# Optimization experiments

Hardware: AMD Instinct MI355X
Metric: run time of the kernel (lower is better)

## Reference

```python
import jax, jax.numpy as jnp
import numpy as np

BATCH = 1_000_000
NUM_KDE = 500_000
RKHS = 20
OUT = 128
NUM_NODES = 100_000


def setup_inputs() -> dict:
    key = jax.random.key(0)
    ks = jax.random.split(key, 9)
    src = jax.random.randint(ks[0], (BATCH,), 0, NUM_NODES, dtype=jnp.int64 if jax.config.read('jax_enable_x64') else jnp.int32)
    dst = jax.random.randint(ks[1], (BATCH,), 0, NUM_NODES, dtype=src.dtype)
    t_diff = jax.random.uniform(ks[2], (BATCH,), dtype=jnp.float32) * 1000.0
    kde_idx = jax.random.randint(ks[3], (BATCH,), 0, NUM_KDE, dtype=src.dtype)
    kde_mask = jax.random.randint(ks[4], (BATCH,), 0, 2) == 1
    kde_table = jax.random.normal(ks[5], (NUM_KDE, RKHS), dtype=jnp.float32)
    W_proj = jax.random.normal(ks[6], (OUT, RKHS), dtype=jnp.float32) * (1.0 / np.sqrt(RKHS))
    b_proj = jnp.zeros((OUT,), dtype=jnp.float32)
    W_fb = jax.random.normal(ks[7], (OUT, 1), dtype=jnp.float32)
    b_fb = jax.random.normal(ks[8], (OUT,), dtype=jnp.float32)
    return {
        'src': src, 'dst': dst, 't_diff': t_diff,
        'kde_idx': kde_idx, 'kde_mask': kde_mask, 'kde_table': kde_table,
        'W_proj': W_proj, 'b_proj': b_proj, 'W_fb': W_fb, 'b_fb': b_fb,
    }


def reference(src, dst, t_diff, kde_idx, kde_mask, kde_table, W_proj, b_proj, W_fb, b_fb):
    # Gather KDE vectors for every edge (miss rows gather a dummy row, masked out below).
    kde_vecs = kde_table[kde_idx]                       # [B, RKHS]
    # rkhs_projection: Linear(RKHS -> OUT)
    kde_out = jnp.einsum('br,or->bo', kde_vecs, W_proj) + b_proj   # [B, OUT]
    # fallback_encoder: cos(Linear(1 -> OUT))
    fb_out = jnp.cos(t_diff[:, None] * W_fb[:, 0][None, :] + b_fb)  # [B, OUT]
    return jnp.where(kde_mask[:, None], kde_out, fb_out)
```

## Files before the change

kernel.cpp:

```cpp
#include <hip/hip_runtime.h>
#include <hip/hip_bf16.h>

#define BATCH_N 1000000
#define RKHS_N 20
#define OUT_N 128
#define ROWS_PER_WAVE 16
#define ROWS_PER_BLOCK 64

__global__ void kde_probe(const unsigned char* __restrict__ mask,
                          const unsigned short* __restrict__ td,
                          unsigned int* __restrict__ cfg)
{
    int i = blockIdx.x * blockDim.x + threadIdx.x;
    unsigned int bits = 0;
    if ((i & 3) != 0 && mask[i] != 0) bits |= 1u;
    if (td[2 * i] & 0x8000u)          bits |= 2u;
    unsigned long long m1 = __ballot(bits & 1u);
    unsigned long long m2 = __ballot(bits & 2u);
    if ((threadIdx.x & 63) == 0) {
        unsigned int v = (m1 ? 1u : 0u) | (m2 ? 2u : 0u);
        if (v) atomicOr(cfg, v);
    }
}

template<bool BF16>
__device__ __forceinline__ float ldf(const void* p, long long i)
{
    if constexpr (BF16) {
        return __bfloat162float(((const __hip_bfloat16*)p)[i]);
    } else {
        return ((const float*)p)[i];
    }
}

template<bool BF16, bool MASK8>
__device__ __forceinline__ void run_impl(const void* __restrict__ t_diff,
                                         const int* __restrict__ kde_idx,
                                         const void* __restrict__ kde_mask,
                                         const void* __restrict__ kde_table,
                                         const void* __restrict__ W_proj,
                                         const void* __restrict__ b_proj,
                                         const void* __restrict__ W_fb,
                                         const void* __restrict__ b_fb,
                                         void* __restrict__ out)
{
    const int tid  = threadIdx.x;
    const int wave = tid >> 6;
    const int lane = tid & 63;
    const int o0   = lane * 2;

    float w0[RKHS_N], w1[RKHS_N];
#pragma unroll
    for (int r = 0; r < RKHS_N; ++r) {
        w0[r] = ldf<BF16>(W_proj, (long long)o0 * RKHS_N + r);
        w1[r] = ldf<BF16>(W_proj, (long long)(o0 + 1) * RKHS_N + r);
    }
    const float bp0 = ldf<BF16>(b_proj, o0), bp1 = ldf<BF16>(b_proj, o0 + 1);
    const float wf0 = ldf<BF16>(W_fb,  o0), wf1 = ldf<BF16>(W_fb,  o0 + 1);
    const float bb0 = ldf<BF16>(b_fb,  o0), bb1 = ldf<BF16>(b_fb,  o0 + 1);

    const long long base = (long long)blockIdx.x * ROWS_PER_BLOCK
                         + (long long)wave * ROWS_PER_WAVE;

    int idxs[ROWS_PER_WAVE];
    int mvs[ROWS_PER_WAVE];
#pragma unroll
    for (int r = 0; r < ROWS_PER_WAVE; ++r) {
        long long b = base + r;
        int idx = kde_idx[b];
        int m = MASK8 ? (int)((const unsigned char*)kde_mask)[b]
                      : ((const int*)kde_mask)[b];
        idxs[r] = __builtin_amdgcn_readfirstlane(idx);
        mvs[r]  = __builtin_amdgcn_readfirstlane(m);
    }

#pragma unroll
    for (int r = 0; r < ROWS_PER_WAVE; ++r) {
        long long b = base + r;
        float2 res;
        if (mvs[r]) {
            long long voff = (long long)idxs[r] * RKHS_N;
            float a0 = bp0, a1 = bp1;
#pragma unroll
            for (int k = 0; k < RKHS_N; ++k) {
                float v = ldf<BF16>(kde_table, voff + k);
                a0 = fmaf(v, w0[k], a0);
                a1 = fmaf(v, w1[k], a1);
            }
            res.x = a0; res.y = a1;
        } else {
            float t = ldf<BF16>(t_diff, b);
            res.x = __cosf(fmaf(t, wf0, bb0));
            res.y = __cosf(fmaf(t, wf1, bb1));
        }
        long long widx = b * (OUT_N / 2) + lane;
        if constexpr (BF16) {
            __hip_bfloat162 pk;
            pk.x = __float2bfloat16(res.x);
            pk.y = __float2bfloat16(res.y);
            unsigned int ub;
            __builtin_memcpy(&ub, &pk, 4);
            __builtin_nontemporal_store(ub, (unsigned int*)out + widx);
        } else {
            unsigned long long uv;
            __builtin_memcpy(&uv, &res, 8);
            __builtin_nontemporal_store(uv, (unsigned long long*)out + widx);
        }
    }
}

__global__ __launch_bounds__(256)
void kde_main(const void* __restrict__ t_diff,
              const int* __restrict__ kde_idx,
              const void* __restrict__ kde_mask,
              const void* __restrict__ kde_table,
              const void* __restrict__ W_proj,
              const void* __restrict__ b_proj,
              const void* __restrict__ W_fb,
              const void* __restrict__ b_fb,
              void* __restrict__ out,
              const unsigned int* __restrict__ cfg)
{
    const unsigned int c = *cfg;
    if (c & 2u) {
        if (c & 1u) run_impl<false, true >(t_diff, kde_idx, kde_mask, kde_table, W_proj, b_proj, W_fb, b_fb, out);
        else        run_impl<false, false>(t_diff, kde_idx, kde_mask, kde_table, W_proj, b_proj, W_fb, b_fb, out);
    } else {
        if (c & 1u) run_impl<true,  true >(t_diff, kde_idx, kde_mask, kde_table, W_proj, b_proj, W_fb, b_fb, out);
        else        run_impl<true,  false>(t_diff, kde_idx, kde_mask, kde_table, W_proj, b_proj, W_fb, b_fb, out);
    }
}

extern "C" void kernel_launch(void* const* d_in, const int* in_sizes, int n_in,
                              void* d_out, int out_size, void* d_ws, size_t ws_size,
                              hipStream_t stream)
{
    const void* t_diff    = d_in[2];
    const int*  kde_idx   = (const int*)d_in[3];
    const void* kde_mask  = d_in[4];
    const void* kde_table = d_in[5];
    const void* W_proj    = d_in[6];
    const void* b_proj    = d_in[7];
    const void* W_fb      = d_in[8];
    const void* b_fb      = d_in[9];

    unsigned int* cfg = (unsigned int*)d_ws;
    hipMemsetAsync(cfg, 0, sizeof(unsigned int), stream);
    kde_probe<<<256, 256, 0, stream>>>((const unsigned char*)kde_mask,
                                       (const unsigned short*)t_diff, cfg);
    kde_main<<<BATCH_N / ROWS_PER_BLOCK, 256, 0, stream>>>(
        t_diff, kde_idx, kde_mask, kde_table, W_proj, b_proj, W_fb, b_fb,
        d_out, cfg);
}
```

Before: 709.0 us.

## Stage KDE row gathers cooperatively through LDS with packed bf16 loads

Instead of each lane redundantly loading all table elements for a row through per-lane scalar loads, each wave gathers its 16 rows' KDE vectors cooperatively as dwords into LDS, then reads them back with vector LDS loads. Mask, t_diff and weights are loaded as packed dwords and unpacked from bf16 by bit shifts. This aims to cut gather latency and load instruction count, but it gathers rows even for masked-out edges and relies on in-wave LDS ordering without a barrier.

```diff
diff --git a/kernel.cpp b/kernel.cpp
--- a/kernel.cpp
+++ b/kernel.cpp
@@ -4,8 +4,10 @@
 #define BATCH_N 1000000
 #define RKHS_N 20
 #define OUT_N 128
-#define ROWS_PER_WAVE 16
-#define ROWS_PER_BLOCK 64
+#define RPW 16
+#define WAVES 4
+#define ROWS_PER_BLOCK (RPW * WAVES)
+#define GRID_N (BATCH_N / ROWS_PER_BLOCK)
 
 __global__ void kde_probe(const unsigned char* __restrict__ mask,
                           const unsigned short* __restrict__ td,
@@ -23,14 +25,11 @@
     }
 }
 
-template<bool BF16>
-__device__ __forceinline__ float ldf(const void* p, long long i)
-{
-    if constexpr (BF16) {
-        return __bfloat162float(((const __hip_bfloat16*)p)[i]);
-    } else {
-        return ((const float*)p)[i];
-    }
+__device__ __forceinline__ float bflo(unsigned int w) {
+    return __uint_as_float(w << 16);
+}
+__device__ __forceinline__ float bfhi(unsigned int w) {
+    return __uint_as_float(w & 0xffff0000u);
 }
 
 template<bool BF16, bool MASK8>
@@ -42,69 +41,126 @@
                                          const void* __restrict__ b_proj,
                                          const void* __restrict__ W_fb,
                                          const void* __restrict__ b_fb,
-                                         void* __restrict__ out)
-{
+                                         void* __restrict__ out,
+                                         unsigned int* __restrict__ lds)
+{
+    constexpr int DW   = BF16 ? 10 : 20;
+    constexpr int LDSW = BF16 ? 12 : 20;
+    constexpr int TOT  = RPW * DW;
+
     const int tid  = threadIdx.x;
     const int wave = tid >> 6;
     const int lane = tid & 63;
-    const int o0   = lane * 2;
+    const int base = blockIdx.x * ROWS_PER_BLOCK + wave * RPW;
 
     float w0[RKHS_N], w1[RKHS_N];
-#pragma unroll
-    for (int r = 0; r < RKHS_N; ++r) {
-        w0[r] = ldf<BF16>(W_proj, (long long)o0 * RKHS_N + r);
-        w1[r] = ldf<BF16>(W_proj, (long long)(o0 + 1) * RKHS_N + r);
-    }
-    const float bp0 = ldf<BF16>(b_proj, o0), bp1 = ldf<BF16>(b_proj, o0 + 1);
-    const float wf0 = ldf<BF16>(W_fb,  o0), wf1 = ldf<BF16>(W_fb,  o0 + 1);
-    const float bb0 = ldf<BF16>(b_fb,  o0), bb1 = ldf<BF16>(b_fb,  o0 + 1);
-
-    const long long base = (long long)blockIdx.x * ROWS_PER_BLOCK
-                         + (long long)wave * ROWS_PER_WAVE;
-
-    int idxs[ROWS_PER_WAVE];
-    int mvs[ROWS_PER_WAVE];
-#pragma unroll
-    for (int r = 0; r < ROWS_PER_WAVE; ++r) {
-        long long b = base + r;
-        int idx = kde_idx[b];
-        int m = MASK8 ? (int)((const unsigned char*)kde_mask)[b]
-                      : ((const int*)kde_mask)[b];
-        idxs[r] = __builtin_amdgcn_readfirstlane(idx);
-        mvs[r]  = __builtin_amdgcn_readfirstlane(m);
-    }
-
-#pragma unroll
-    for (int r = 0; r < ROWS_PER_WAVE; ++r) {
-        long long b = base + r;
-        float2 res;
-        if (mvs[r]) {
-            long long voff = (long long)idxs[r] * RKHS_N;
+    float bp0, bp1, wf0, wf1, bb0, bb1;
+    if constexpr (BF16) {
+        const unsigned int* wp = (const unsigned int*)W_proj;
+#pragma unroll
+        for (int d = 0; d < 10; ++d) {
+            unsigned int a = wp[lane * 20 + d];
+            unsigned int b = wp[lane * 20 + 10 + d];
+            w0[2 * d] = bflo(a); w0[2 * d + 1] = bfhi(a);
+            w1[2 * d] = bflo(b); w1[2 * d + 1] = bfhi(b);
+        }
+        unsigned int v;
+        v = ((const unsigned int*)b_proj)[lane]; bp0 = bflo(v); bp1 = bfhi(v);
+        v = ((const unsigned int*)W_fb)[lane];   wf0 = bflo(v); wf1 = bfhi(v);
+        v = ((const unsigned int*)b_fb)[lane];   bb0 = bflo(v); bb1 = bfhi(v);
+    } else {
+        const float* wp = (const float*)W_proj;
+#pragma unroll
+        for (int k = 0; k < RKHS_N; ++k) {
+            w0[k] = wp[(2 * lane) * RKHS_N + k];
+            w1[k] = wp[(2 * lane + 1) * RKHS_N + k];
+        }
+        bp0 = ((const float*)b_proj)[2 * lane]; bp1 = ((const float*)b_proj)[2 * lane + 1];
+        wf0 = ((const float*)W_fb)[2 * lane];   wf1 = ((const float*)W_fb)[2 * lane + 1];
+        bb0 = ((const float*)b_fb)[2 * lane];   bb1 = ((const float*)b_fb)[2 * lane + 1];
+    }
+
+    unsigned int* wl = lds + wave * (RPW * LDSW);
+    const unsigned int* tbl = (const unsigned int*)kde_table;
+    constexpr int ITERS = (TOT + 63) / 64;
+#pragma unroll
+    for (int i = 0; i < ITERS; ++i) {
+        int j = lane + 64 * i;
+        if ((TOT % 64 == 0) || (j < TOT)) {
+            int r = j / DW;
+            int d = j - r * DW;
+            int idx = kde_idx[base + r];
+            wl[r * LDSW + d] = tbl[(size_t)(unsigned)idx * DW + d];
+        }
+    }
+
+    const unsigned int* mp = (const unsigned int*)kde_mask;
+    const unsigned int* tp = (const unsigned int*)t_diff;
+#pragma unroll
+    for (int r = 0; r < RPW; ++r) {
+        unsigned int m;
+        if constexpr (MASK8)
+            m = (mp[(base >> 2) + (r >> 2)] >> ((r & 3) * 8)) & 0xffu;
+        else
+            m = mp[base + r];
+
+        float rx, ry;
+        if (m) {
             float a0 = bp0, a1 = bp1;
-#pragma unroll
-            for (int k = 0; k < RKHS_N; ++k) {
-                float v = ldf<BF16>(kde_table, voff + k);
-                a0 = fmaf(v, w0[k], a0);
-                a1 = fmaf(v, w1[k], a1);
+            const unsigned int* rowp = wl + r * LDSW;
+            if constexpr (BF16) {
+                uint4 q0 = *(const uint4*)(rowp);
+                uint4 q1 = *(const uint4*)(rowp + 4);
+                uint2 q2 = *(const uint2*)(rowp + 8);
+                unsigned int dwv[10] = {q0.x, q0.y, q0.z, q0.w,
+                                        q1.x, q1.y, q1.z, q1.w,
+                                        q2.x, q2.y};
+#pragma unroll
+                for (int d = 0; d < 10; ++d) {
+                    float v0 = bflo(dwv[d]), v1 = bfhi(dwv[d]);
+                    a0 = fmaf(v0, w0[2 * d], a0);
+                    a1 = fmaf(v0, w1[2 * d], a1);
+                    a0 = fmaf(v1, w0[2 * d + 1], a0);
+                    a1 = fmaf(v1, w1[2 * d + 1], a1);
+                }
+            } else {
+                uint4 q[5];
+#pragma unroll
+                for (int i5 = 0; i5 < 5; ++i5) q[i5] = *(const uint4*)(rowp + 4 * i5);
+                const unsigned int* dv = (const unsigned int*)q;
+#pragma unroll
+                for (int k = 0; k < RKHS_N; ++k) {
+                    float v = __uint_as_float(dv[k]);
+                    a0 = fmaf(v, w0[k], a0);
+                    a1 = fmaf(v, w1[k], a1);
+                }
             }
-            res.x = a0; res.y = a1;
+            rx = a0; ry = a1;
         } else {
-            float t = ldf<BF16>(t_diff, b);
-            res.x = __cosf(fmaf(t, wf0, bb0));
-            res.y = __cosf(fmaf(t, wf1, bb1));
-        }
-        long long widx = b * (OUT_N / 2) + lane;
+            float t;
+            if constexpr (BF16) {
+                unsigned int w = tp[(base >> 1) + (r >> 1)];
+                t = (r & 1) ? bfhi(w) : bflo(w);
+            } else {
+                t = ((const float*)t_diff)[base + r];
+            }
+            rx = __cosf(fmaf(t, wf0, bb0));
+            ry = __cosf(fmaf(t, wf1, bb1));
+        }
+
+        size_t g = (size_t)(base + r);
         if constexpr (BF16) {
             __hip_bfloat162 pk;
-            pk.x = __float2bfloat16(res.x);
-            pk.y = __float2bfloat16(res.y);
+            pk.x = __float2bfloat16(rx);
+            pk.y = __float2bfloat16(ry);
             unsigned int ub;
             __builtin_memcpy(&ub, &pk, 4);
-            __builtin_nontemporal_store(ub, (unsigned int*)out + widx);
+            __builtin_nontemporal_store(ub, (unsigned int*)out + g * 64 + lane);
         } else {
+            float2 fv; fv.x = rx; fv.y = ry;
             unsigned long long uv;
-            __builtin_memcpy(&uv, &res, 8);
-            __builtin_nontemporal_store(uv, (unsigned long long*)out + widx);
+            __builtin_memcpy(&uv, &fv, 8);
+            __builtin_nontemporal_store(uv, (unsigned long long*)out + g * 64 + lane);
         }
     }
 }
@@ -121,13 +177,14 @@
               void* __restrict__ out,
               const unsigned int* __restrict__ cfg)
 {
+    __shared__ unsigned int lds[WAVES * RPW * 20];
     const unsigned int c = *cfg;
     if (c & 2u) {
-        if (c & 1u) run_impl<false, true >(t_diff, kde_idx, kde_mask, kde_table, W_proj, b_proj, W_fb, b_fb, out);
-        else        run_impl<false, false>(t_diff, kde_idx, kde_mask, kde_table, W_proj, b_proj, W_fb, b_fb, out);
+        if (c & 1u) run_impl<false, true >(t_diff, kde_idx, kde_mask, kde_table, W_proj, b_proj, W_fb, b_fb, out, lds);
+        else        run_impl<false, false>(t_diff, kde_idx, kde_mask, kde_table, W_proj, b_proj, W_fb, b_fb, out, lds);
     } else {
-        if (c & 1u) run_impl<true,  true >(t_diff, kde_idx, kde_mask, kde_table, W_proj, b_proj, W_fb, b_fb, out);
-        else        run_impl<true,  false>(t_diff, kde_idx, kde_mask, kde_table, W_proj, b_proj, W_fb, b_fb, out);
+        if (c & 1u) run_impl<true,  true >(t_diff, kde_idx, kde_mask, kde_table, W_proj, b_proj, W_fb, b_fb, out, lds);
+        else        run_impl<true,  false>(t_diff, kde_idx, kde_mask, kde_table, W_proj, b_proj, W_fb, b_fb, out, lds);
     }
 }
 
@@ -148,7 +205,7 @@
     hipMemsetAsync(cfg, 0, sizeof(unsigned int), stream);
     kde_probe<<<256, 256, 0, stream>>>((const unsigned char*)kde_mask,
                                        (const unsigned short*)t_diff, cfg);
-    kde_main<<<BATCH_N / ROWS_PER_BLOCK, 256, 0, stream>>>(
+    kde_main<<<GRID_N, 256, 0, stream>>>(
         t_diff, kde_idx, kde_mask, kde_table, W_proj, b_proj, W_fb, b_fb,
         d_out, cfg);
 }
```

Measured after the change: 657.5 us. 7.3% less time.
